# Kernel tuning notes

Measured on AMD Instinct MI355X. Metric: run time of the kernel, lower is better.

The kernel has to match this reference:

```python
import jax, jax.numpy as jnp
import numpy as np

N = 100000      # nodes
E = 2500000     # edges
DIN, H, DOUT = 3, 32, 4
EPS = 1e-5

def _lin(k, i, o):
    kw, kb = jax.random.split(k)
    lim = 1.0 / np.sqrt(i)
    W = jax.random.uniform(kw, (i, o), jnp.float32, -lim, lim)
    b = jax.random.uniform(kb, (o,), jnp.float32, -lim, lim)
    return W, b

def setup_inputs():
    key = jax.random.key(0)
    ks = jax.random.split(key, 12)
    x = jax.random.normal(ks[0], (N, DIN), jnp.float32)
    edge_index = jax.random.randint(ks[1], (2, E), 0, N, dtype=jnp.int32)
    w_in1, b_in1 = _lin(ks[2], DIN, H)
    w_in2, b_in2 = _lin(ks[3], H, H)
    gamma = jnp.ones((H,), jnp.float32)
    beta = jnp.zeros((H,), jnp.float32)
    wg1, bg1 = _lin(ks[4], H, H)
    wg2, bg2 = _lin(ks[5], H, H)
    wg3, bg3 = _lin(ks[6], H, H)
    wo1, bo1 = _lin(ks[7], H, H)
    wo2, bo2 = _lin(ks[8], H, H)
    wo3, bo3 = _lin(ks[9], H, DOUT)
    return dict(x=x, w_in1=w_in1, b_in1=b_in1, w_in2=w_in2, b_in2=b_in2,
                gamma=gamma, beta=beta,
                wg1=wg1, bg1=bg1, wg2=wg2, bg2=bg2, wg3=wg3, bg3=bg3,
                wo1=wo1, bo1=bo1, wo2=wo2, bo2=bo2, wo3=wo3, bo3=bo3,
                edge_index=edge_index)

def _gcn(h, W, b, src, dst, norm):
    # PyG GCNConv: x' = scatter_add(norm * (xW)[src] -> dst) + bias
    hw = h @ W                                   # [N, H]
    msg = hw[src] * norm[:, None]                # [E+N, H] gather + scale
    out = jax.ops.segment_sum(msg, dst, num_segments=N)
    return out + b

def reference(x, w_in1, b_in1, w_in2, b_in2, gamma, beta,
              wg1, bg1, wg2, bg2, wg3, bg3,
              wo1, bo1, wo2, bo2, wo3, bo3, edge_index):
    leaky = lambda v: jax.nn.leaky_relu(v, 0.01)
    # input MLP
    h = leaky(x @ w_in1 + b_in1)
    h = leaky(h @ w_in2 + b_in2)
    # BatchNorm1d (training-mode batch statistics, biased variance)
    mu = jnp.mean(h, axis=0)
    var = jnp.mean((h - mu) ** 2, axis=0)
    h = (h - mu) * jax.lax.rsqrt(var + EPS) * gamma + beta
    # gcn_norm with self-loops: deg over target index, sym normalization
    loop = jnp.arange(N, dtype=edge_index.dtype)
    src = jnp.concatenate([edge_index[0], loop])
    dst = jnp.concatenate([edge_index[1], loop])
    deg = jax.ops.segment_sum(jnp.ones_like(src, jnp.float32), dst, num_segments=N)
    dis = jax.lax.rsqrt(deg)                     # deg >= 1 due to self-loops
    norm = dis[src] * dis[dst]                   # [E+N]
    h = jax.nn.elu(_gcn(h, wg1, bg1, src, dst, norm))
    h = jax.nn.elu(_gcn(h, wg2, bg2, src, dst, norm))
    h = jax.nn.elu(_gcn(h, wg3, bg3, src, dst, norm))
    # output MLP
    r = leaky(h @ wo1 + bo1)
    r = leaky(r @ wo2 + bo2)
    r = r @ wo3 + bo3                            # [N, 4]
    r = r.at[:, 0].set(jax.nn.sigmoid(r[:, 0]))
    return r
```

## Files before the change

kernel.cpp:

```cpp
#include <hip/hip_runtime.h>
#include <hip/hip_fp16.h>

#define HF 32
#define EPS 1e-5f
#define BSH 7
#define BSZ 128
#define CH  4096
#define SUBCAP 512
#define CAP (8*SUBCAP)

typedef int vi4 __attribute__((ext_vector_type(4)));

__device__ __forceinline__ float leaky(float v){ return fmaxf(v, 0.01f*v); }
__device__ __forceinline__ float elu1(float v){ return v > 0.f ? v : (expf(v)-1.f); }
__device__ __forceinline__ float sigmoidf(float v){ return 1.f/(1.f+expf(-v)); }

__device__ __forceinline__ int4 nt_load_i4(const int* p){
    vi4 v = __builtin_nontemporal_load((const vi4*)p);
    return make_int4(v.x, v.y, v.z, v.w);
}

__device__ __forceinline__ void addrow8(float* a, float4 v){
    const __half2* p = (const __half2*)&v;
#pragma unroll
    for (int k = 0; k < 4; k++){
        float2 f = __half22float2(p[k]);
        a[2*k] += f.x; a[2*k+1] += f.y;
    }
}
__device__ __forceinline__ float4 h2add4f(float4 a, float4 b){
    __half2* pa = (__half2*)&a; __half2* pb = (__half2*)&b;
    float4 r; __half2* pr = (__half2*)&r;
#pragma unroll
    for (int k = 0; k < 4; k++) pr[k] = __hadd2(pa[k], pb[k]);
    return r;
}

union SMem {
    struct {
        float sW1[3*HF]; float sB1[HF]; float sW2[HF*HF]; float sB2[HF];
        float sh[256][33];
    } mlp;
    struct { int lcnt[1024]; int lbase[1024]; int lpos[1024]; } bin;
};

__global__ __launch_bounds__(256)
void k_mlp_bin(const float* __restrict__ x,
               const float* __restrict__ w1, const float* __restrict__ b1,
               const float* __restrict__ w2, const float* __restrict__ b2,
               __half* __restrict__ h, float* __restrict__ stats,
               const int* __restrict__ src, const int* __restrict__ dst,
               int* __restrict__ gfill, int* __restrict__ ep,
               int N, int E, int B, int NC){
    __shared__ SMem sm;
    int t = threadIdx.x;
    if ((int)blockIdx.x < NC){
        int bid = blockIdx.x;
        for (int i = t; i < B; i += 256){ sm.bin.lcnt[i] = 0; sm.bin.lpos[i] = 0; }
        __syncthreads();
        int base = bid * CH;
        int xcd = bid & 7;
        int dv[16], sv[16];
        if (base + CH <= E){
#pragma unroll
            for (int i = 0; i < 4; i++){
                int4 d4 = nt_load_i4(dst + base + (t + i*256)*4);
                int4 s4 = nt_load_i4(src + base + (t + i*256)*4);
                dv[4*i]   = d4.x; dv[4*i+1] = d4.y; dv[4*i+2] = d4.z; dv[4*i+3] = d4.w;
                sv[4*i]   = s4.x; sv[4*i+1] = s4.y; sv[4*i+2] = s4.z; sv[4*i+3] = s4.w;
            }
        } else {
#pragma unroll
            for (int i = 0; i < 16; i++){
                int e = base + t + i*256;
                dv[i] = (e < E) ? dst[e] : -1;
                sv[i] = (e < E) ? src[e] : 0;
            }
        }
#pragma unroll
        for (int i = 0; i < 16; i++)
            if (dv[i] >= 0) atomicAdd(&sm.bin.lcnt[dv[i] >> BSH], 1);
        __syncthreads();
        for (int i = t; i < B; i += 256){
            int c = sm.bin.lcnt[i];
            sm.bin.lbase[i] = c ? (i*CAP + xcd*SUBCAP + atomicAdd(&gfill[i*8 + xcd], c)) : 0;
        }
        __syncthreads();
#pragma unroll
        for (int i = 0; i < 16; i++)
            if (dv[i] >= 0){
                int bb = dv[i] >> BSH;
                int p = sm.bin.lbase[bb] + atomicAdd(&sm.bin.lpos[bb], 1);
                ep[p] = (sv[i] << BSH) | (dv[i] & (BSZ-1));
            }
    } else {
        for (int i = t; i < 3*HF; i += 256) sm.mlp.sW1[i] = w1[i];
        if (t < HF){ sm.mlp.sB1[t] = b1[t]; sm.mlp.sB2[t] = b2[t]; }
        for (int i = t; i < HF*HF; i += 256) sm.mlp.sW2[i] = w2[i];
        __syncthreads();
        int n = (blockIdx.x - NC)*256 + t;
        float h2[HF];
        if (n < N){
            float x0 = x[(size_t)n*3], x1 = x[(size_t)n*3+1], x2 = x[(size_t)n*3+2];
            float h1[HF];
#pragma unroll
            for (int j = 0; j < HF; j++){
                float v = fmaf(x0, sm.mlp.sW1[j], fmaf(x1, sm.mlp.sW1[HF+j],
                          fmaf(x2, sm.mlp.sW1[2*HF+j], sm.mlp.sB1[j])));
                h1[j] = leaky(v);
            }
#pragma unroll
            for (int j = 0; j < HF; j++){
                float v = sm.mlp.sB2[j];
#pragma unroll
                for (int i = 0; i < HF; i++) v = fmaf(h1[i], sm.mlp.sW2[i*HF+j], v);
                h2[j] = leaky(v);
            }
            float4* hv = (float4*)(h + (size_t)n*HF);
#pragma unroll
            for (int jb = 0; jb < 4; jb++){
                __half2 hh[4];
#pragma unroll
                for (int k = 0; k < 4; k++)
                    hh[k] = __float22half2_rn(make_float2(h2[jb*8+2*k], h2[jb*8+2*k+1]));
                hv[jb] = *(float4*)hh;
            }
        } else {
#pragma unroll
            for (int j = 0; j < HF; j++) h2[j] = 0.f;
        }
#pragma unroll
        for (int j = 0; j < HF; j++) sm.mlp.sh[t][j] = h2[j];
        __syncthreads();
        int f = t & 31, g = t >> 5;
        float s = 0.f, ss = 0.f;
        for (int i = 0; i < 32; i++){
            float v = sm.mlp.sh[g*32 + i][f];
            s += v; ss += v*v;
        }
        __syncthreads();
        sm.mlp.sh[g][f] = s; sm.mlp.sh[8+g][f] = ss;
        __syncthreads();
        if (t < HF){
            float a = 0.f, b = 0.f;
#pragma unroll
            for (int g2 = 0; g2 < 8; g2++){ a += sm.mlp.sh[g2][t]; b += sm.mlp.sh[8+g2][t]; }
            atomicAdd(&stats[t], a);
            atomicAdd(&stats[HF+t], b);
        }
    }
}

__global__ __launch_bounds__(256)
void k_csr_t1(int* __restrict__ ep, const int* __restrict__ gfill,
              int2* __restrict__ rowp2, float* __restrict__ dis,
              const __half* __restrict__ h, const float* __restrict__ stats,
              const float* __restrict__ gamma, const float* __restrict__ beta,
              const float* __restrict__ W, __half* __restrict__ tout,
              int N, int B){
    __shared__ int sep[CAP];
    __shared__ int lcnt[128], lpre[128], lfill[128];
    __shared__ float sW[HF*HF];
    __shared__ float sscale[HF], sshift[HF];
    int t = threadIdx.x;
    int b = blockIdx.x;
    for (int i = t; i < HF*HF; i += 256) sW[i] = W[i];
    if (t < HF){
        float inv = 1.0f/(float)N;
        float mu  = stats[t]*inv;
        float var = stats[HF+t]*inv - mu*mu;
        float rs  = rsqrtf(var + EPS);
        float sc  = rs*gamma[t];
        sscale[t] = sc;
        sshift[t] = beta[t] - mu*sc;
    }
    if (t < 128){ lcnt[t] = 0; lfill[t] = 0; }
    int cx[8], coff[8], cnt = 0;
#pragma unroll
    for (int xx = 0; xx < 8; xx++){ cx[xx] = gfill[b*8 + xx]; coff[xx] = cnt; cnt += cx[xx]; }
    int base = b*CAP;
    __syncthreads();
#pragma unroll
    for (int xx = 0; xx < 8; xx++)
        for (int j = t; j < cx[xx]; j += 256) sep[coff[xx] + j] = ep[base + xx*SUBCAP + j];
    __syncthreads();
    for (int e = t; e < cnt; e += 256) atomicAdd(&lcnt[sep[e] & (BSZ-1)], 1);
    __syncthreads();
    if (t < 128){
        int dg = lcnt[t];
        int pre = 0;
        for (int j = 0; j < t; j++) pre += lcnt[j];
        lpre[t] = pre;
        int n = b*BSZ + t;
        if (n < N){
            rowp2[n] = make_int2(base + pre, base + pre + dg);
            dis[n]   = rsqrtf((float)dg + 1.0f);
        }
    }
    __syncthreads();
    for (int e = t; e < cnt; e += 256){
        int val = sep[e];
        int d = val & (BSZ-1);
        int p = lpre[d] + atomicAdd(&lfill[d], 1);
        ep[base + p] = val >> BSH;
    }
    int nloc = t >> 1, fh = (t & 1) * 16;
    int n = b*BSZ + nloc;
    if (n < N){
        float dloc = rsqrtf((float)lcnt[nloc] + 1.0f);
        const float4* hv4 = (const float4*)h + (size_t)n*4;
        float v[HF];
#pragma unroll
        for (int k = 0; k < 4; k++){
            float4 raw = hv4[k];
            const __half2* p2 = (const __half2*)&raw;
#pragma unroll
            for (int q = 0; q < 4; q++){
                float2 f2 = __half22float2(p2[q]);
                v[8*k + 2*q]     = f2.x;
                v[8*k + 2*q + 1] = f2.y;
            }
        }
#pragma unroll
        for (int f = 0; f < HF; f++) v[f] = fmaf(v[f], sscale[f], sshift[f]);
        float o[16];
#pragma unroll
        for (int j = 0; j < 16; j++) o[j] = 0.f;
#pragma unroll
        for (int i = 0; i < HF; i++){
            float vi = v[i];
#pragma unroll
            for (int j4 = 0; j4 < 4; j4++){
                float4 w4 = *(const float4*)&sW[i*HF + fh + 4*j4];
                o[4*j4]   = fmaf(vi, w4.x, o[4*j4]);
                o[4*j4+1] = fmaf(vi, w4.y, o[4*j4+1]);
                o[4*j4+2] = fmaf(vi, w4.z, o[4*j4+2]);
                o[4*j4+3] = fmaf(vi, w4.w, o[4*j4+3]);
            }
        }
        float4* ov = (float4*)tout + (size_t)n*4 + (t & 1)*2;
#pragma unroll
        for (int k = 0; k < 2; k++){
            __half2 hh[4];
#pragma unroll
            for (int q = 0; q < 4; q++)
                hh[q] = __float22half2_rn(make_float2(o[8*k+2*q]*dloc, o[8*k+2*q+1]*dloc));
            ov[k] = *(float4*)hh;
        }
    }
}

__global__ __launch_bounds__(256)
void k_gather_t(const __half* __restrict__ tin, const int* __restrict__ esrc,
                const int2* __restrict__ rowp2, const float* __restrict__ dis,
                const float* __restrict__ bias, const float* __restrict__ W,
                __half* __restrict__ tout, int N){
    __shared__ float sW[HF*HF];
    __shared__ float sh[32][33];
    int tid = threadIdx.x;
    for (int i = tid; i < HF*HF; i += 256) sW[i] = W[i];
    int node = tid >> 3, l2 = tid & 7, l = l2 & 3, hf = l2 >> 2;
    int n = blockIdx.x*32 + node;
    float acc[8] = {0.f,0.f,0.f,0.f,0.f,0.f,0.f,0.f};
    float d = 0.f;
    const float4* tv = (const float4*)tin;
    if (n < N){
        if (hf == 0) addrow8(acc, tv[(size_t)n*4 + l]);
        int2 r = rowp2[n];
        int e0 = r.x, e1 = r.y;
        int ea = (e0 + 3) & ~3; if (ea > e1) ea = e1;
        if (hf == 0) for (int e = e0; e < ea; e++) addrow8(acc, tv[(size_t)esrc[e]*4 + l]);
        int nch = (e1 - ea) >> 2;
        int c = hf;
        for (; c + 2 < nch; c += 4){
            int4 a4 = nt_load_i4(&esrc[ea + 4*c]);
            int4 b4 = nt_load_i4(&esrc[ea + 4*(c+2)]);
            float4 v0 = tv[(size_t)a4.x*4 + l];
            float4 v1 = tv[(size_t)a4.y*4 + l];
            float4 v2 = tv[(size_t)a4.z*4 + l];
            float4 v3 = tv[(size_t)a4.w*4 + l];
            float4 v4 = tv[(size_t)b4.x*4 + l];
            float4 v5 = tv[(size_t)b4.y*4 + l];
            float4 v6 = tv[(size_t)b4.z*4 + l];
            float4 v7 = tv[(size_t)b4.w*4 + l];
            addrow8(acc, h2add4f(h2add4f(v0, v1), h2add4f(v2, v3)));
            addrow8(acc, h2add4f(h2add4f(v4, v5), h2add4f(v6, v7)));
        }
        for (; c < nch; c += 2){
            int4 s4 = nt_load_i4(&esrc[ea + 4*c]);
            float4 v0 = tv[(size_t)s4.x*4 + l];
            float4 v1 = tv[(size_t)s4.y*4 + l];
            float4 v2 = tv[(size_t)s4.z*4 + l];
            float4 v3 = tv[(size_t)s4.w*4 + l];
            addrow8(acc, h2add4f(h2add4f(v0, v1), h2add4f(v2, v3)));
        }
        if (hf == 1) for (int e = ea + 4*nch; e < e1; e++) addrow8(acc, tv[(size_t)esrc[e]*4 + l]);
#pragma unroll
        for (int cc = 0; cc < 8; cc++) acc[cc] += __shfl_xor(acc[cc], 4);
        d = dis[n];
#pragma unroll
        for (int cc = 0; cc < 8; cc++)
            acc[cc] = elu1(fmaf(d, acc[cc], bias[8*l + cc]));
    }
    __syncthreads();
    if (hf == 0){
#pragma unroll
        for (int cc = 0; cc < 8; cc++) sh[node][8*l + cc] = acc[cc];
    }
    __syncthreads();
    float o[4] = {0.f,0.f,0.f,0.f};
#pragma unroll
    for (int i = 0; i < HF; i++){
        float hvv = sh[node][i];
        float4 w4 = *(const float4*)&sW[i*HF + 4*l2];
        o[0] = fmaf(hvv, w4.x, o[0]); o[1] = fmaf(hvv, w4.y, o[1]);
        o[2] = fmaf(hvv, w4.z, o[2]); o[3] = fmaf(hvv, w4.w, o[3]);
    }
    if (n < N){
        __half2 hh[2];
        hh[0] = __float22half2_rn(make_float2(o[0]*d, o[1]*d));
        hh[1] = __float22half2_rn(make_float2(o[2]*d, o[3]*d));
        ((float2*)tout)[(size_t)n*8 + l2] = *(float2*)hh;
    }
}

__global__ __launch_bounds__(256)
void k_gather_out(const __half* __restrict__ tin, const int* __restrict__ esrc,
                  const int2* __restrict__ rowp2, const float* __restrict__ dis,
                  const float* __restrict__ bg3,
                  const float* __restrict__ wo1, const float* __restrict__ bo1,
                  const float* __restrict__ wo2, const float* __restrict__ bo2,
                  const float* __restrict__ wo3, const float* __restrict__ bo3,
                  float* __restrict__ out, int N){
    __shared__ float sW1[HF*HF], sW2[HF*HF], sW3[HF*4];
    __shared__ float sh[32][33], sh2[32][33];
    int tid = threadIdx.x;
    for (int i = tid; i < HF*HF; i += 256){ sW1[i] = wo1[i]; sW2[i] = wo2[i]; }
    if (tid < HF*4) sW3[tid] = wo3[tid];
    int node = tid >> 3, l2 = tid & 7, l = l2 & 3, hf = l2 >> 2;
    int n = blockIdx.x*32 + node;
    float acc[8] = {0.f,0.f,0.f,0.f,0.f,0.f,0.f,0.f};
    const float4* tv = (const float4*)tin;
    if (n < N){
        if (hf == 0) addrow8(acc, tv[(size_t)n*4 + l]);
        int2 r = rowp2[n];
        int e0 = r.x, e1 = r.y;
        int ea = (e0 + 3) & ~3; if (ea > e1) ea = e1;
        if (hf == 0) for (int e = e0; e < ea; e++) addrow8(acc, tv[(size_t)esrc[e]*4 + l]);
        int nch = (e1 - ea) >> 2;
        int c = hf;
        for (; c + 2 < nch; c += 4){
            int4 a4 = nt_load_i4(&esrc[ea + 4*c]);
            int4 b4 = nt_load_i4(&esrc[ea + 4*(c+2)]);
            float4 v0 = tv[(size_t)a4.x*4 + l];
            float4 v1 = tv[(size_t)a4.y*4 + l];
            float4 v2 = tv[(size_t)a4.z*4 + l];
            float4 v3 = tv[(size_t)a4.w*4 + l];
            float4 v4 = tv[(size_t)b4.x*4 + l];
            float4 v5 = tv[(size_t)b4.y*4 + l];
            float4 v6 = tv[(size_t)b4.z*4 + l];
            float4 v7 = tv[(size_t)b4.w*4 + l];
            addrow8(acc, h2add4f(h2add4f(v0, v1), h2add4f(v2, v3)));
            addrow8(acc, h2add4f(h2add4f(v4, v5), h2add4f(v6, v7)));
        }
        for (; c < nch; c += 2){
            int4 s4 = nt_load_i4(&esrc[ea + 4*c]);
            float4 v0 = tv[(size_t)s4.x*4 + l];
            float4 v1 = tv[(size_t)s4.y*4 + l];
            float4 v2 = tv[(size_t)s4.z*4 + l];
            float4 v3 = tv[(size_t)s4.w*4 + l];
            addrow8(acc, h2add4f(h2add4f(v0, v1), h2add4f(v2, v3)));
        }
        if (hf == 1) for (int e = ea + 4*nch; e < e1; e++) addrow8(acc, tv[(size_t)esrc[e]*4 + l]);
#pragma unroll
        for (int cc = 0; cc < 8; cc++) acc[cc] += __shfl_xor(acc[cc], 4);
        float d = dis[n];
#pragma unroll
        for (int cc = 0; cc < 8; cc++)
            acc[cc] = elu1(fmaf(d, acc[cc], bg3[8*l + cc]));
    }
    __syncthreads();
    if (hf == 0){
#pragma unroll
        for (int cc = 0; cc < 8; cc++) sh[node][8*l + cc] = acc[cc];
    }
    __syncthreads();
    float o1[4];
#pragma unroll
    for (int cc = 0; cc < 4; cc++) o1[cc] = bo1[4*l2 + cc];
#pragma unroll
    for (int i = 0; i < HF; i++){
        float hvv = sh[node][i];
        float4 w4 = *(const float4*)&sW1[i*HF + 4*l2];
        o1[0] = fmaf(hvv, w4.x, o1[0]); o1[1] = fmaf(hvv, w4.y, o1[1]);
        o1[2] = fmaf(hvv, w4.z, o1[2]); o1[3] = fmaf(hvv, w4.w, o1[3]);
    }
#pragma unroll
    for (int cc = 0; cc < 4; cc++) sh2[node][4*l2 + cc] = leaky(o1[cc]);
    __syncthreads();
    float o2[4];
#pragma unroll
    for (int cc = 0; cc < 4; cc++) o2[cc] = bo2[4*l2 + cc];
#pragma unroll
    for (int i = 0; i < HF; i++){
        float hvv = sh2[node][i];
        float4 w4 = *(const float4*)&sW2[i*HF + 4*l2];
        o2[0] = fmaf(hvv, w4.x, o2[0]); o2[1] = fmaf(hvv, w4.y, o2[1]);
        o2[2] = fmaf(hvv, w4.z, o2[2]); o2[3] = fmaf(hvv, w4.w, o2[3]);
    }
    __syncthreads();
#pragma unroll
    for (int cc = 0; cc < 4; cc++) sh[node][4*l2 + cc] = leaky(o2[cc]);
    __syncthreads();
    if (n < N && l2 < 4){
        float v = bo3[l2];
#pragma unroll
        for (int i = 0; i < HF; i++) v = fmaf(sh[node][i], sW3[i*4 + l2], v);
        if (l2 == 0) v = sigmoidf(v);
        out[(size_t)n*4 + l2] = v;
    }
}

extern "C" void kernel_launch(void* const* d_in, const int* in_sizes, int n_in,
                              void* d_out, int out_size, void* d_ws, size_t ws_size,
                              hipStream_t stream) {
    const float* x     = (const float*)d_in[0];
    const float* w_in1 = (const float*)d_in[1];
    const float* b_in1 = (const float*)d_in[2];
    const float* w_in2 = (const float*)d_in[3];
    const float* b_in2 = (const float*)d_in[4];
    const float* gamma = (const float*)d_in[5];
    const float* beta  = (const float*)d_in[6];
    const float* wg1   = (const float*)d_in[7];
    const float* bg1   = (const float*)d_in[8];
    const float* wg2   = (const float*)d_in[9];
    const float* bg2   = (const float*)d_in[10];
    const float* wg3   = (const float*)d_in[11];
    const float* bg3   = (const float*)d_in[12];
    const float* wo1   = (const float*)d_in[13];
    const float* bo1   = (const float*)d_in[14];
    const float* wo2   = (const float*)d_in[15];
    const float* bo2   = (const float*)d_in[16];
    const float* wo3   = (const float*)d_in[17];
    const float* bo3   = (const float*)d_in[18];
    const int*   ei    = (const int*)d_in[19];

    int N = in_sizes[0] / 3;
    int E = in_sizes[19] / 2;
    int B = (N + BSZ - 1) >> BSH;

    char* w = (char*)d_ws;
    size_t o = 0;
    auto alloc = [&](size_t bytes){ size_t r = o; o = (o + bytes + 255) & ~(size_t)255; return r; };
    float* stats = (float*)(w + alloc(2*HF*sizeof(float)));
    int*   gfill = (int*)  (w + alloc((size_t)B*8*4));
    size_t zero_bytes = o;
    int2*  rowp2 = (int2*) (w + alloc((size_t)N*8));
    float* dis   = (float*)(w + alloc((size_t)N*4));
    int*   ep    = (int*)  (w + alloc((size_t)B*CAP*4));
    __half* bufH = (__half*)(w + alloc((size_t)N*HF*2));
    __half* tA   = (__half*)(w + alloc((size_t)N*HF*2));
    __half* tB   = (__half*)(w + alloc((size_t)N*HF*2));

    hipMemsetAsync(d_ws, 0, zero_bytes, stream);

    const int* src = ei;
    const int* dst = ei + E;
    int NB1 = (N + 255) / 256;
    int NC  = (E + CH - 1) / CH;
    int GN  = (N + 31) / 32;

    k_mlp_bin<<<NC + NB1, 256, 0, stream>>>(x, w_in1, b_in1, w_in2, b_in2, bufH, stats,
                                            src, dst, gfill, ep, N, E, B, NC);
    k_csr_t1<<<B, 256, 0, stream>>>(ep, gfill, rowp2, dis,
                                    bufH, stats, gamma, beta, wg1, tA, N, B);
    k_gather_t<<<GN, 256, 0, stream>>>(tA, ep, rowp2, dis, bg1, wg2, tB, N);
    k_gather_t<<<GN, 256, 0, stream>>>(tB, ep, rowp2, dis, bg2, wg3, tA, N);
    k_gather_out<<<GN, 256, 0, stream>>>(tA, ep, rowp2, dis, bg3,
                                         wo1, bo1, wo2, bo2, wo3, bo3, (float*)d_out, N);
}
```

Before: 286.4 us.

## Enlarge binning chunks, reorder MLP/bin blocks, prefetch edge indices in gathers

After: 291.9 us. No clear change (+1.9%).

```diff
diff --git a/kernel.cpp b/kernel.cpp
--- a/kernel.cpp
+++ b/kernel.cpp
@@ -5,7 +5,7 @@
 #define EPS 1e-5f
 #define BSH 7
 #define BSZ 128
-#define CH  4096
+#define CH  16384
 #define SUBCAP 512
 #define CAP (8*SUBCAP)
 
@@ -51,54 +51,15 @@
                __half* __restrict__ h, float* __restrict__ stats,
                const int* __restrict__ src, const int* __restrict__ dst,
                int* __restrict__ gfill, int* __restrict__ ep,
-               int N, int E, int B, int NC){
+               int N, int E, int B, int NB1){
     __shared__ SMem sm;
     int t = threadIdx.x;
-    if ((int)blockIdx.x < NC){
-        int bid = blockIdx.x;
-        for (int i = t; i < B; i += 256){ sm.bin.lcnt[i] = 0; sm.bin.lpos[i] = 0; }
-        __syncthreads();
-        int base = bid * CH;
-        int xcd = bid & 7;
-        int dv[16], sv[16];
-        if (base + CH <= E){
-#pragma unroll
-            for (int i = 0; i < 4; i++){
-                int4 d4 = nt_load_i4(dst + base + (t + i*256)*4);
-                int4 s4 = nt_load_i4(src + base + (t + i*256)*4);
-                dv[4*i]   = d4.x; dv[4*i+1] = d4.y; dv[4*i+2] = d4.z; dv[4*i+3] = d4.w;
-                sv[4*i]   = s4.x; sv[4*i+1] = s4.y; sv[4*i+2] = s4.z; sv[4*i+3] = s4.w;
-            }
-        } else {
-#pragma unroll
-            for (int i = 0; i < 16; i++){
-                int e = base + t + i*256;
-                dv[i] = (e < E) ? dst[e] : -1;
-                sv[i] = (e < E) ? src[e] : 0;
-            }
-        }
-#pragma unroll
-        for (int i = 0; i < 16; i++)
-            if (dv[i] >= 0) atomicAdd(&sm.bin.lcnt[dv[i] >> BSH], 1);
-        __syncthreads();
-        for (int i = t; i < B; i += 256){
-            int c = sm.bin.lcnt[i];
-            sm.bin.lbase[i] = c ? (i*CAP + xcd*SUBCAP + atomicAdd(&gfill[i*8 + xcd], c)) : 0;
-        }
-        __syncthreads();
-#pragma unroll
-        for (int i = 0; i < 16; i++)
-            if (dv[i] >= 0){
-                int bb = dv[i] >> BSH;
-                int p = sm.bin.lbase[bb] + atomicAdd(&sm.bin.lpos[bb], 1);
-                ep[p] = (sv[i] << BSH) | (dv[i] & (BSZ-1));
-            }
-    } else {
+    if ((int)blockIdx.x < NB1){
         for (int i = t; i < 3*HF; i += 256) sm.mlp.sW1[i] = w1[i];
         if (t < HF){ sm.mlp.sB1[t] = b1[t]; sm.mlp.sB2[t] = b2[t]; }
         for (int i = t; i < HF*HF; i += 256) sm.mlp.sW2[i] = w2[i];
         __syncthreads();
-        int n = (blockIdx.x - NC)*256 + t;
+        int n = blockIdx.x*256 + t;
         float h2[HF];
         if (n < N){
             float x0 = x[(size_t)n*3], x1 = x[(size_t)n*3+1], x2 = x[(size_t)n*3+2];
@@ -147,6 +108,58 @@
             for (int g2 = 0; g2 < 8; g2++){ a += sm.mlp.sh[g2][t]; b += sm.mlp.sh[8+g2][t]; }
             atomicAdd(&stats[t], a);
             atomicAdd(&stats[HF+t], b);
+        }
+    } else {
+        int bid = blockIdx.x - NB1;
+        for (int i = t; i < B; i += 256){ sm.bin.lcnt[i] = 0; sm.bin.lpos[i] = 0; }
+        __syncthreads();
+        int base = bid * CH;
+        int xcd = blockIdx.x & 7;
+        bool full = (base + CH <= E);
+        if (full){
+            for (int i = 0; i < 16; i++){
+                int4 d4 = nt_load_i4(dst + base + (t + i*256)*4);
+                atomicAdd(&sm.bin.lcnt[d4.x >> BSH], 1);
+                atomicAdd(&sm.bin.lcnt[d4.y >> BSH], 1);
+                atomicAdd(&sm.bin.lcnt[d4.z >> BSH], 1);
+                atomicAdd(&sm.bin.lcnt[d4.w >> BSH], 1);
+            }
+        } else {
+            for (int i = 0; i < 64; i++){
+                int e = base + t + i*256;
+                if (e < E) atomicAdd(&sm.bin.lcnt[dst[e] >> BSH], 1);
+            }
+        }
+        __syncthreads();
+        for (int i = t; i < B; i += 256){
+            int c = sm.bin.lcnt[i];
+            sm.bin.lbase[i] = c ? (i*CAP + xcd*SUBCAP + atomicAdd(&gfill[i*8 + xcd], c)) : 0;
+        }
+        __syncthreads();
+        if (full){
+            for (int i = 0; i < 16; i++){
+                int idx = base + (t + i*256)*4;
+                int4 d4 = *(const int4*)(dst + idx);
+                int4 s4 = *(const int4*)(src + idx);
+                int dd[4] = {d4.x, d4.y, d4.z, d4.w};
+                int ss[4] = {s4.x, s4.y, s4.z, s4.w};
+#pragma unroll
+                for (int k = 0; k < 4; k++){
+                    int bb = dd[k] >> BSH;
+                    int p = sm.bin.lbase[bb] + atomicAdd(&sm.bin.lpos[bb], 1);
+                    ep[p] = (ss[k] << BSH) | (dd[k] & (BSZ-1));
+                }
+            }
+        } else {
+            for (int i = 0; i < 64; i++){
+                int e = base + t + i*256;
+                if (e < E){
+                    int d = dst[e], s = src[e];
+                    int bb = d >> BSH;
+                    int p = sm.bin.lbase[bb] + atomicAdd(&sm.bin.lpos[bb], 1);
+                    ep[p] = (s << BSH) | (d & (BSZ-1));
+                }
+            }
         }
     }
 }
@@ -272,19 +285,31 @@
         if (hf == 0) for (int e = e0; e < ea; e++) addrow8(acc, tv[(size_t)esrc[e]*4 + l]);
         int nch = (e1 - ea) >> 2;
         int c = hf;
-        for (; c + 2 < nch; c += 4){
+        if (c + 2 < nch){
             int4 a4 = nt_load_i4(&esrc[ea + 4*c]);
             int4 b4 = nt_load_i4(&esrc[ea + 4*(c+2)]);
-            float4 v0 = tv[(size_t)a4.x*4 + l];
-            float4 v1 = tv[(size_t)a4.y*4 + l];
-            float4 v2 = tv[(size_t)a4.z*4 + l];
-            float4 v3 = tv[(size_t)a4.w*4 + l];
-            float4 v4 = tv[(size_t)b4.x*4 + l];
-            float4 v5 = tv[(size_t)b4.y*4 + l];
-            float4 v6 = tv[(size_t)b4.z*4 + l];
-            float4 v7 = tv[(size_t)b4.w*4 + l];
-            addrow8(acc, h2add4f(h2add4f(v0, v1), h2add4f(v2, v3)));
-            addrow8(acc, h2add4f(h2add4f(v4, v5), h2add4f(v6, v7)));
+            while (true){
+                int cn = c + 4;
+                bool more = (cn + 2 < nch);
+                int4 na4, nb4;
+                if (more){
+                    na4 = nt_load_i4(&esrc[ea + 4*cn]);
+                    nb4 = nt_load_i4(&esrc[ea + 4*(cn+2)]);
+                }
+                float4 v0 = tv[(size_t)a4.x*4 + l];
+                float4 v1 = tv[(size_t)a4.y*4 + l];
+                float4 v2 = tv[(size_t)a4.z*4 + l];
+                float4 v3 = tv[(size_t)a4.w*4 + l];
+                float4 v4 = tv[(size_t)b4.x*4 + l];
+                float4 v5 = tv[(size_t)b4.y*4 + l];
+                float4 v6 = tv[(size_t)b4.z*4 + l];
+                float4 v7 = tv[(size_t)b4.w*4 + l];
+                addrow8(acc, h2add4f(h2add4f(v0, v1), h2add4f(v2, v3)));
+                addrow8(acc, h2add4f(h2add4f(v4, v5), h2add4f(v6, v7)));
+                c = cn;
+                if (!more) break;
+                a4 = na4; b4 = nb4;
+            }
         }
         for (; c < nch; c += 2){
             int4 s4 = nt_load_i4(&esrc[ea + 4*c]);
@@ -349,19 +374,31 @@
         if (hf == 0) for (int e = e0; e < ea; e++) addrow8(acc, tv[(size_t)esrc[e]*4 + l]);
         int nch = (e1 - ea) >> 2;
         int c = hf;
-        for (; c + 2 < nch; c += 4){
+        if (c + 2 < nch){
             int4 a4 = nt_load_i4(&esrc[ea + 4*c]);
             int4 b4 = nt_load_i4(&esrc[ea + 4*(c+2)]);
-            float4 v0 = tv[(size_t)a4.x*4 + l];
-            float4 v1 = tv[(size_t)a4.y*4 + l];
-            float4 v2 = tv[(size_t)a4.z*4 + l];
-            float4 v3 = tv[(size_t)a4.w*4 + l];
-            float4 v4 = tv[(size_t)b4.x*4 + l];
-            float4 v5 = tv[(size_t)b4.y*4 + l];
-            float4 v6 = tv[(size_t)b4.z*4 + l];
-            float4 v7 = tv[(size_t)b4.w*4 + l];
-            addrow8(acc, h2add4f(h2add4f(v0, v1), h2add4f(v2, v3)));
-            addrow8(acc, h2add4f(h2add4f(v4, v5), h2add4f(v6, v7)));
+            while (true){
+                int cn = c + 4;
+                bool more = (cn + 2 < nch);
+                int4 na4, nb4;
+                if (more){
+                    na4 = nt_load_i4(&esrc[ea + 4*cn]);
+                    nb4 = nt_load_i4(&esrc[ea + 4*(cn+2)]);
+                }
+                float4 v0 = tv[(size_t)a4.x*4 + l];
+                float4 v1 = tv[(size_t)a4.y*4 + l];
+                float4 v2 = tv[(size_t)a4.z*4 + l];
+                float4 v3 = tv[(size_t)a4.w*4 + l];
+                float4 v4 = tv[(size_t)b4.x*4 + l];
+                float4 v5 = tv[(size_t)b4.y*4 + l];
+                float4 v6 = tv[(size_t)b4.z*4 + l];
+                float4 v7 = tv[(size_t)b4.w*4 + l];
+                addrow8(acc, h2add4f(h2add4f(v0, v1), h2add4f(v2, v3)));
+                addrow8(acc, h2add4f(h2add4f(v4, v5), h2add4f(v6, v7)));
+                c = cn;
+                if (!more) break;
+                a4 = na4; b4 = nb4;
+            }
         }
         for (; c < nch; c += 2){
             int4 s4 = nt_load_i4(&esrc[ea + 4*c]);
@@ -470,8 +507,8 @@
     int NC  = (E + CH - 1) / CH;
     int GN  = (N + 31) / 32;
 
-    k_mlp_bin<<<NC + NB1, 256, 0, stream>>>(x, w_in1, b_in1, w_in2, b_in2, bufH, stats,
-                                            src, dst, gfill, ep, N, E, B, NC);
+    k_mlp_bin<<<NB1 + NC, 256, 0, stream>>>(x, w_in1, b_in1, w_in2, b_in2, bufH, stats,
+                                            src, dst, gfill, ep, N, E, B, NB1);
     k_csr_t1<<<B, 256, 0, stream>>>(ep, gfill, rowp2, dis,
                                     bufH, stats, gamma, beta, wg1, tA, N, B);
     k_gather_t<<<GN, 256, 0, stream>>>(tA, ep, rowp2, dis, bg1, wg2, tB, N);
```
